# Kernel tuning notes

Measured on AMD Instinct MI355X. Metric: run time of the kernel, lower is better.

## Reference

```python
import jax, jax.numpy as jnp
import numpy as np

NUM_NODES = 10000
NUM_EDGES = 640000
INPUT_DIM = 128
HIDDEN_DIM = 128


def setup_inputs() -> dict:
    key = jax.random.key(0)
    k_x, k_e, k_w1, k_b1, k_w2, k_b2 = jax.random.split(key, 6)
    x = jax.random.normal(k_x, (NUM_NODES, INPUT_DIM), dtype=jnp.float32)
    edge_index = jax.random.randint(k_e, (NUM_EDGES, 2), 0, NUM_NODES, dtype=jnp.int64)
    # MLP params (torch Linear: y = x @ W.T + b; store W already transposed as [in, out])
    s1 = 1.0 / np.sqrt(INPUT_DIM)
    s2 = 1.0 / np.sqrt(HIDDEN_DIM)
    W1 = jax.random.uniform(k_w1, (INPUT_DIM, HIDDEN_DIM), jnp.float32, -s1, s1)
    b1 = jax.random.uniform(k_b1, (HIDDEN_DIM,), jnp.float32, -s1, s1)
    W2 = jax.random.uniform(k_w2, (HIDDEN_DIM, HIDDEN_DIM), jnp.float32, -s2, s2)
    b2 = jax.random.uniform(k_b2, (HIDDEN_DIM,), jnp.float32, -s2, s2)
    return {"x": x, "edge_index": edge_index, "W1": W1, "b1": b1, "W2": W2, "b2": b2}


def reference(x, edge_index, W1, b1, W2, b2):
    # GIN aggregation: sum of neighbor features along edges (row <- col) + self loop.
    row = edge_index[:, 0]
    col = edge_index[:, 1]
    # scatter-add gathered neighbor features into destination nodes
    agg = jax.ops.segment_sum(x[col], row, num_segments=NUM_NODES)
    agg = agg + x  # self-loop contribution (identity edges appended in torch code)
    # 2-layer MLP: Linear -> ReLU -> Linear
    h = jnp.maximum(agg @ W1 + b1, 0.0)
    return h @ W2 + b2
```

## Files before the change

kernel.cpp:

```cpp
#include <hip/hip_runtime.h>

#define NN   10000
#define NE   640000
#define DIM  128
#define NTILES (NN / 16)
#define NBIN  320
#define CAPB  4096
#define EPB   2048
#define FILL_BLOCKS ((NE + EPB - 1) / EPB)
#define CLCAP 512
#define PREP_ITEMS 193088

typedef __attribute__((ext_vector_type(8))) short bf16x8;
typedef __attribute__((ext_vector_type(8))) unsigned short u16x8;
typedef __attribute__((ext_vector_type(4))) float f32x4;

__device__ inline unsigned short f2bf(float f) {
    unsigned u = __builtin_bit_cast(unsigned, f);
    unsigned r = (u + 0x7fffu + ((u >> 16) & 1u)) >> 16;
    return (unsigned short)r;
}
__device__ inline float bf2f(unsigned short u) {
    return __builtin_bit_cast(float, (unsigned)u << 16);
}

#define OFF_BINMEM 1280
#define OFF_XB     5244160
#define OFF_W1P    7804160
#define OFF_W2P    7836928
#define WS_NEED    7869696

__global__ __launch_bounds__(256) void prep_kernel(
        const float* __restrict__ W1, const float* __restrict__ W2,
        const float* __restrict__ x,
        unsigned short* __restrict__ W1p, unsigned short* __restrict__ W2p,
        unsigned short* __restrict__ xb, int* __restrict__ bincnt) {
    int id = blockIdx.x * 256 + threadIdx.x;
    if (id < 32768) {
        const float* W = (id < 16384) ? W1 : W2;
        unsigned short* Wp = (id < 16384) ? W1p : W2p;
        int f = id & 16383;
        int e = f & 7, lane = (f >> 3) & 63, kt = (f >> 9) & 3, nt = f >> 11;
        int kglob = kt * 32 + (lane >> 4) * 8 + e;
        int jglob = nt * 16 + (lane & 15);
        Wp[f] = f2bf(W[kglob * DIM + jglob]);
    } else if (id < 33088) {
        bincnt[id - 32768] = 0;
    } else if (id < PREP_ITEMS) {
        int i = (id - 33088) * 8;
        float4 a = *reinterpret_cast<const float4*>(x + i);
        float4 b = *reinterpret_cast<const float4*>(x + i + 4);
        u16x8 pk;
        pk[0] = f2bf(a.x); pk[1] = f2bf(a.y); pk[2] = f2bf(a.z); pk[3] = f2bf(a.w);
        pk[4] = f2bf(b.x); pk[5] = f2bf(b.y); pk[6] = f2bf(b.z); pk[7] = f2bf(b.w);
        *reinterpret_cast<u16x8*>(xb + i) = pk;
    }
}

__global__ __launch_bounds__(256) void binfill_kernel(
        const int* __restrict__ ei, int* __restrict__ bincnt,
        unsigned* __restrict__ binmem) {
    __shared__ int hist[NBIN];
    __shared__ int base_s[NBIN];
    const int t = threadIdx.x;
    for (int b = t; b < NBIN; b += 256) hist[b] = 0;
    __syncthreads();

    unsigned pk[8];
    int bn[8], rk[8];
    const int e0 = blockIdx.x * EPB;
    #pragma unroll
    for (int i = 0; i < 8; ++i) {
        int idx = e0 + i * 256 + t;
        bn[i] = -1;
        if (idx < NE) {
            int2 rc = *reinterpret_cast<const int2*>(ei + 2 * idx);
            bn[i] = rc.x >> 5;
            pk[i] = ((unsigned)(rc.x & 31) << 14) | (unsigned)rc.y;
            rk[i] = atomicAdd(&hist[bn[i]], 1);
        }
    }
    __syncthreads();
    for (int b = t; b < NBIN; b += 256) {
        int h = hist[b];
        base_s[b] = (h > 0) ? atomicAdd(&bincnt[b], h) : 0;
    }
    __syncthreads();
    #pragma unroll
    for (int i = 0; i < 8; ++i) {
        if (bn[i] >= 0) {
            int pos = base_s[bn[i]] + rk[i];
            if (pos < CAPB)
                binmem[(size_t)bn[i] * CAPB + pos] = pk[i];
        }
    }
}

__global__ __launch_bounds__(256) void gather_mlp_kernel(
        const unsigned short* __restrict__ xb,
        const int* __restrict__ bincnt,
        const unsigned* __restrict__ binmem,
        const unsigned short* __restrict__ W1p,
        const unsigned short* __restrict__ W2p,
        const float* __restrict__ b1,
        const float* __restrict__ b2,
        float* __restrict__ out) {
    __shared__ __align__(16) unsigned short aggs[16][136];
    __shared__ __align__(16) unsigned short hbuf[16][136];
    __shared__ __align__(16) unsigned short clist[16][CLCAP];
    __shared__ int lcnt[16];

    const int row0 = blockIdx.x * 16;
    const int t = threadIdx.x;

    if (t < 16) lcnt[t] = 0;
    __syncthreads();
    {
        const int bin  = blockIdx.x >> 1;
        const int half = blockIdx.x & 1;
        int bc = bincnt[bin];
        bc = (bc > CAPB) ? CAPB : bc;
        const unsigned* bm = binmem + (size_t)bin * CAPB;
        for (int k = t; k < bc; k += 256) {
            unsigned p = bm[k];
            int rl = p >> 14;
            if ((rl >> 4) == half) {
                int n = rl & 15;
                int slot = atomicAdd(&lcnt[n], 1);
                if (slot < CLCAP)
                    clist[n][slot] = (unsigned short)(p & 0x3FFFu);
            }
        }
    }
    __syncthreads();

    {
        const int n = t >> 4, l = t & 15;
        int deg = lcnt[n];
        deg = (deg > CLCAP) ? CLCAP : deg;
        const size_t lo = l * 8;

        float a0[8], a1[8], a2[8], a3[8];
        {
            u16x8 v = *reinterpret_cast<const u16x8*>(xb + (size_t)(row0 + n) * DIM + lo);
            #pragma unroll
            for (int j = 0; j < 8; ++j) { a0[j] = bf2f(v[j]); a1[j] = 0.f; a2[j] = 0.f; a3[j] = 0.f; }
        }
        int k = 0;
        for (; k + 4 <= deg; k += 4) {
            int c0 = clist[n][k + 0];
            int c1 = clist[n][k + 1];
            int c2 = clist[n][k + 2];
            int c3 = clist[n][k + 3];
            u16x8 v0 = *reinterpret_cast<const u16x8*>(xb + (size_t)c0 * DIM + lo);
            u16x8 v1 = *reinterpret_cast<const u16x8*>(xb + (size_t)c1 * DIM + lo);
            u16x8 v2 = *reinterpret_cast<const u16x8*>(xb + (size_t)c2 * DIM + lo);
            u16x8 v3 = *reinterpret_cast<const u16x8*>(xb + (size_t)c3 * DIM + lo);
            #pragma unroll
            for (int j = 0; j < 8; ++j) {
                a0[j] += bf2f(v0[j]);
                a1[j] += bf2f(v1[j]);
                a2[j] += bf2f(v2[j]);
                a3[j] += bf2f(v3[j]);
            }
        }
        for (; k < deg; ++k) {
            int c = clist[n][k];
            u16x8 v = *reinterpret_cast<const u16x8*>(xb + (size_t)c * DIM + lo);
            #pragma unroll
            for (int j = 0; j < 8; ++j) a0[j] += bf2f(v[j]);
        }
        u16x8 pk;
        #pragma unroll
        for (int j = 0; j < 8; ++j) pk[j] = f2bf((a0[j] + a1[j]) + (a2[j] + a3[j]));
        *reinterpret_cast<u16x8*>(&aggs[n][l * 8]) = pk;
    }
    __syncthreads();

    const int wid  = t >> 6;
    const int lane = t & 63;
    const int r16  = lane & 15;
    const int kg   = lane >> 4;
    const int drow = kg * 4;

    bf16x8 af[4];
    #pragma unroll
    for (int kt = 0; kt < 4; ++kt)
        af[kt] = *reinterpret_cast<const bf16x8*>(&aggs[r16][kt * 32 + kg * 8]);

    const f32x4 zero = {0.f, 0.f, 0.f, 0.f};
    f32x4 acc1[2] = {zero, zero};
    #pragma unroll
    for (int kt = 0; kt < 4; ++kt) {
        #pragma unroll
        for (int q = 0; q < 2; ++q) {
            int nt = wid * 2 + q;
            bf16x8 w = *reinterpret_cast<const bf16x8*>(
                W1p + ((nt * 4 + kt) * 64 + lane) * 8);
            acc1[q] = __builtin_amdgcn_mfma_f32_16x16x32_bf16(af[kt], w, acc1[q], 0, 0, 0);
        }
    }
    #pragma unroll
    for (int q = 0; q < 2; ++q) {
        int nt = wid * 2 + q;
        float bv = b1[nt * 16 + r16];
        #pragma unroll
        for (int r = 0; r < 4; ++r) {
            float h = fmaxf(acc1[q][r] + bv, 0.0f);
            hbuf[drow + r][nt * 16 + r16] = f2bf(h);
        }
    }
    __syncthreads();

    bf16x8 hf[4];
    #pragma unroll
    for (int kt = 0; kt < 4; ++kt)
        hf[kt] = *reinterpret_cast<const bf16x8*>(&hbuf[r16][kt * 32 + kg * 8]);

    f32x4 acc2[2] = {zero, zero};
    #pragma unroll
    for (int kt = 0; kt < 4; ++kt) {
        #pragma unroll
        for (int q = 0; q < 2; ++q) {
            int nt = wid * 2 + q;
            bf16x8 w = *reinterpret_cast<const bf16x8*>(
                W2p + ((nt * 4 + kt) * 64 + lane) * 8);
            acc2[q] = __builtin_amdgcn_mfma_f32_16x16x32_bf16(hf[kt], w, acc2[q], 0, 0, 0);
        }
    }
    #pragma unroll
    for (int q = 0; q < 2; ++q) {
        int nt = wid * 2 + q;
        float bv = b2[nt * 16 + r16];
        #pragma unroll
        for (int r = 0; r < 4; ++r)
            out[(size_t)(row0 + drow + r) * DIM + nt * 16 + r16] = acc2[q][r] + bv;
    }
}

__global__ void fb_zero_kernel(int* __restrict__ p, int n) {
    int i = blockIdx.x * blockDim.x + threadIdx.x;
    if (i < n) p[i] = 0;
}
__global__ void fb_count_kernel(const int* __restrict__ ei, int* __restrict__ deg) {
    int e = blockIdx.x * blockDim.x + threadIdx.x;
    if (e < NE) atomicAdd(&deg[ei[2 * e]], 1);
}
__global__ __launch_bounds__(1024) void fb_scan_kernel(const int* __restrict__ deg,
                                                       int* __restrict__ rowptr) {
    __shared__ int wtot[16];
    const int t = threadIdx.x;
    const int base = t * 10;
    int local[10];
    int s = 0;
    #pragma unroll
    for (int i = 0; i < 10; ++i) {
        int v = (base + i < NN) ? deg[base + i] : 0;
        local[i] = s;
        s += v;
    }
    const int mySum = s;
    #pragma unroll
    for (int off = 1; off < 64; off <<= 1) {
        int v = __shfl_up(s, (unsigned)off, 64);
        if ((t & 63) >= off) s += v;
    }
    if ((t & 63) == 63) wtot[t >> 6] = s;
    __syncthreads();
    if (t == 0) {
        int run = 0;
        #pragma unroll
        for (int i = 0; i < 16; ++i) { int v = wtot[i]; wtot[i] = run; run += v; }
    }
    __syncthreads();
    const int ex = wtot[t >> 6] + (s - mySum);
    #pragma unroll
    for (int i = 0; i < 10; ++i)
        if (base + i < NN) rowptr[base + i] = ex + local[i];
    if (t == 1023) rowptr[NN] = ex + mySum;
}
__global__ void fb_fill_kernel(const int* __restrict__ ei, const int* __restrict__ rowptr,
                               int* __restrict__ fill, int* __restrict__ colidx) {
    int e = blockIdx.x * blockDim.x + threadIdx.x;
    if (e < NE) {
        int r = ei[2 * e], c = ei[2 * e + 1];
        colidx[rowptr[r] + atomicAdd(&fill[r], 1)] = c;
    }
}
__global__ __launch_bounds__(128) void fb_gather_kernel(const float* __restrict__ x,
                                                        const int* __restrict__ rowptr,
                                                        const int* __restrict__ colidx,
                                                        float* __restrict__ agg) {
    const int n = blockIdx.x, j = threadIdx.x;
    const int s = rowptr[n], e = rowptr[n + 1];
    float acc = x[(size_t)n * DIM + j];
    float a0 = 0.f, a1 = 0.f, a2 = 0.f, a3 = 0.f;
    int k = s;
    for (; k + 4 <= e; k += 4) {
        a0 += x[(size_t)colidx[k + 0] * DIM + j];
        a1 += x[(size_t)colidx[k + 1] * DIM + j];
        a2 += x[(size_t)colidx[k + 2] * DIM + j];
        a3 += x[(size_t)colidx[k + 3] * DIM + j];
    }
    for (; k < e; ++k) acc += x[(size_t)colidx[k] * DIM + j];
    agg[(size_t)n * DIM + j] = acc + (a0 + a1) + (a2 + a3);
}
__global__ __launch_bounds__(512) void fb_mlp_kernel(
        const float* __restrict__ agg,
        const float* __restrict__ W1, const float* __restrict__ b1,
        const float* __restrict__ W2, const float* __restrict__ b2,
        float* __restrict__ out) {
    __shared__ float w1s[DIM * DIM];
    __shared__ float w2s[DIM * DIM];
    __shared__ float b1s[DIM], b2s[DIM];
    __shared__ float as[4][DIM], hs[4][DIM];
    for (int i = threadIdx.x; i < DIM * DIM; i += blockDim.x) { w1s[i] = W1[i]; w2s[i] = W2[i]; }
    if (threadIdx.x < DIM) { b1s[threadIdx.x] = b1[threadIdx.x]; b2s[threadIdx.x] = b2[threadIdx.x]; }
    __syncthreads();
    const int r = threadIdx.x >> 7, j = threadIdx.x & 127;
    for (int base = blockIdx.x * 4; base < NN; base += gridDim.x * 4) {
        int rowid = base + r;
        as[r][j] = (rowid < NN) ? agg[(size_t)rowid * DIM + j] : 0.0f;
        __syncthreads();
        float acc = b1s[j];
        #pragma unroll 8
        for (int k = 0; k < DIM; ++k) acc = fmaf(as[r][k], w1s[k * DIM + j], acc);
        hs[r][j] = fmaxf(acc, 0.0f);
        __syncthreads();
        float acc2 = b2s[j];
        #pragma unroll 8
        for (int k = 0; k < DIM; ++k) acc2 = fmaf(hs[r][k], w2s[k * DIM + j], acc2);
        if (rowid < NN) out[(size_t)rowid * DIM + j] = acc2;
        __syncthreads();
    }
}

extern "C" void kernel_launch(void* const* d_in, const int* in_sizes, int n_in,
                              void* d_out, int out_size, void* d_ws, size_t ws_size,
                              hipStream_t stream) {
    const float* x  = (const float*)d_in[0];
    const int*   ei = (const int*)d_in[1];
    const float* W1 = (const float*)d_in[2];
    const float* b1 = (const float*)d_in[3];
    const float* W2 = (const float*)d_in[4];
    const float* b2 = (const float*)d_in[5];
    float* out = (float*)d_out;

    if (ws_size >= WS_NEED) {
        char* ws = (char*)d_ws;
        int* bincnt = (int*)ws;
        unsigned* binmem = (unsigned*)(ws + OFF_BINMEM);
        unsigned short* xb  = (unsigned short*)(ws + OFF_XB);
        unsigned short* W1p = (unsigned short*)(ws + OFF_W1P);
        unsigned short* W2p = (unsigned short*)(ws + OFF_W2P);

        prep_kernel<<<(PREP_ITEMS + 255) / 256, 256, 0, stream>>>(
            W1, W2, x, W1p, W2p, xb, bincnt);
        binfill_kernel<<<FILL_BLOCKS, 256, 0, stream>>>(ei, bincnt, binmem);
        gather_mlp_kernel<<<NTILES, 256, 0, stream>>>(
            xb, bincnt, binmem, W1p, W2p, b1, b2, out);
    } else {
        int* wsI    = (int*)d_ws;
        int* deg    = wsI;
        int* fillc  = wsI + 10240;
        int* rowptr = wsI + 20480;
        int* colidx = wsI + 30720;
        const size_t csr_bytes = (size_t)(30720 + NE) * sizeof(int);
        const size_t agg_bytes = (size_t)NN * DIM * sizeof(float);
        float* agg = (ws_size >= csr_bytes + agg_bytes)
                         ? (float*)((char*)d_ws + csr_bytes) : out;

        fb_zero_kernel<<<(20480 + 255) / 256, 256, 0, stream>>>(deg, 20480);
        fb_count_kernel<<<(NE + 255) / 256, 256, 0, stream>>>(ei, deg);
        fb_scan_kernel<<<1, 1024, 0, stream>>>(deg, rowptr);
        fb_fill_kernel<<<(NE + 255) / 256, 256, 0, stream>>>(ei, rowptr, fillc, colidx);
        fb_gather_kernel<<<NN, 128, 0, stream>>>(x, rowptr, colidx, agg);
        fb_mlp_kernel<<<256, 512, 0, stream>>>(agg, W1, b1, W2, b2, out);
    }
}
```

Before: 41.72 us.

## Merge x-to-bf16 conversion into binning kernel, enlarge edges per bin block

```diff
diff --git a/kernel.cpp b/kernel.cpp
--- a/kernel.cpp
+++ b/kernel.cpp
@@ -6,10 +6,12 @@
 #define NTILES (NN / 16)
 #define NBIN  320
 #define CAPB  4096
-#define EPB   2048
+#define EPB   8192
 #define FILL_BLOCKS ((NE + EPB - 1) / EPB)
+#define CONV_THREADS 160000
+#define CONV_BLOCKS ((CONV_THREADS + 255) / 256)
 #define CLCAP 512
-#define PREP_ITEMS 193088
+#define ZW_ITEMS (32768 + NBIN)
 
 typedef __attribute__((ext_vector_type(8))) short bf16x8;
 typedef __attribute__((ext_vector_type(8))) unsigned short u16x8;
@@ -30,11 +32,10 @@
 #define OFF_W2P    7836928
 #define WS_NEED    7869696
 
-__global__ __launch_bounds__(256) void prep_kernel(
+__global__ __launch_bounds__(256) void zw_kernel(
         const float* __restrict__ W1, const float* __restrict__ W2,
-        const float* __restrict__ x,
         unsigned short* __restrict__ W1p, unsigned short* __restrict__ W2p,
-        unsigned short* __restrict__ xb, int* __restrict__ bincnt) {
+        int* __restrict__ bincnt) {
     int id = blockIdx.x * 256 + threadIdx.x;
     if (id < 32768) {
         const float* W = (id < 16384) ? W1 : W2;
@@ -44,54 +45,53 @@
         int kglob = kt * 32 + (lane >> 4) * 8 + e;
         int jglob = nt * 16 + (lane & 15);
         Wp[f] = f2bf(W[kglob * DIM + jglob]);
-    } else if (id < 33088) {
+    } else if (id < ZW_ITEMS) {
         bincnt[id - 32768] = 0;
-    } else if (id < PREP_ITEMS) {
-        int i = (id - 33088) * 8;
-        float4 a = *reinterpret_cast<const float4*>(x + i);
-        float4 b = *reinterpret_cast<const float4*>(x + i + 4);
-        u16x8 pk;
-        pk[0] = f2bf(a.x); pk[1] = f2bf(a.y); pk[2] = f2bf(a.z); pk[3] = f2bf(a.w);
-        pk[4] = f2bf(b.x); pk[5] = f2bf(b.y); pk[6] = f2bf(b.z); pk[7] = f2bf(b.w);
-        *reinterpret_cast<u16x8*>(xb + i) = pk;
-    }
-}
-
-__global__ __launch_bounds__(256) void binfill_kernel(
-        const int* __restrict__ ei, int* __restrict__ bincnt,
-        unsigned* __restrict__ binmem) {
-    __shared__ int hist[NBIN];
-    __shared__ int base_s[NBIN];
+    }
+}
+
+__global__ __launch_bounds__(256) void build_kernel(
+        const int* __restrict__ ei, const float* __restrict__ x,
+        int* __restrict__ bincnt, unsigned* __restrict__ binmem,
+        unsigned short* __restrict__ xb) {
     const int t = threadIdx.x;
-    for (int b = t; b < NBIN; b += 256) hist[b] = 0;
-    __syncthreads();
-
-    unsigned pk[8];
-    int bn[8], rk[8];
-    const int e0 = blockIdx.x * EPB;
-    #pragma unroll
-    for (int i = 0; i < 8; ++i) {
-        int idx = e0 + i * 256 + t;
-        bn[i] = -1;
-        if (idx < NE) {
-            int2 rc = *reinterpret_cast<const int2*>(ei + 2 * idx);
-            bn[i] = rc.x >> 5;
-            pk[i] = ((unsigned)(rc.x & 31) << 14) | (unsigned)rc.y;
-            rk[i] = atomicAdd(&hist[bn[i]], 1);
-        }
-    }
-    __syncthreads();
-    for (int b = t; b < NBIN; b += 256) {
-        int h = hist[b];
-        base_s[b] = (h > 0) ? atomicAdd(&bincnt[b], h) : 0;
-    }
-    __syncthreads();
-    #pragma unroll
-    for (int i = 0; i < 8; ++i) {
-        if (bn[i] >= 0) {
-            int pos = base_s[bn[i]] + rk[i];
-            if (pos < CAPB)
-                binmem[(size_t)bn[i] * CAPB + pos] = pk[i];
+    if (blockIdx.x < FILL_BLOCKS) {
+        __shared__ int hist[NBIN];
+        for (int b = t; b < NBIN; b += 256) hist[b] = 0;
+        __syncthreads();
+        const int e0 = blockIdx.x * EPB;
+        for (int i = 0; i < EPB / 256; ++i) {
+            int idx = e0 + i * 256 + t;
+            if (idx < NE)
+                atomicAdd(&hist[ei[2 * idx] >> 5], 1);
+        }
+        __syncthreads();
+        for (int b = t; b < NBIN; b += 256) {
+            int h = hist[b];
+            hist[b] = (h > 0) ? atomicAdd(&bincnt[b], h) : 0;
+        }
+        __syncthreads();
+        for (int i = 0; i < EPB / 256; ++i) {
+            int idx = e0 + i * 256 + t;
+            if (idx < NE) {
+                int2 rc = *reinterpret_cast<const int2*>(ei + 2 * idx);
+                int bn = rc.x >> 5;
+                int pos = atomicAdd(&hist[bn], 1);
+                if (pos < CAPB)
+                    binmem[(size_t)bn * CAPB + pos] =
+                        ((unsigned)(rc.x & 31) << 14) | (unsigned)rc.y;
+            }
+        }
+    } else {
+        int pid = (blockIdx.x - FILL_BLOCKS) * 256 + t;
+        if (pid < CONV_THREADS) {
+            int i = pid * 8;
+            float4 a = *reinterpret_cast<const float4*>(x + i);
+            float4 b = *reinterpret_cast<const float4*>(x + i + 4);
+            u16x8 pk;
+            pk[0] = f2bf(a.x); pk[1] = f2bf(a.y); pk[2] = f2bf(a.z); pk[3] = f2bf(a.w);
+            pk[4] = f2bf(b.x); pk[5] = f2bf(b.y); pk[6] = f2bf(b.z); pk[7] = f2bf(b.w);
+            *reinterpret_cast<u16x8*>(xb + i) = pk;
         }
     }
 }
@@ -354,9 +354,10 @@
         unsigned short* W1p = (unsigned short*)(ws + OFF_W1P);
         unsigned short* W2p = (unsigned short*)(ws + OFF_W2P);
 
-        prep_kernel<<<(PREP_ITEMS + 255) / 256, 256, 0, stream>>>(
-            W1, W2, x, W1p, W2p, xb, bincnt);
-        binfill_kernel<<<FILL_BLOCKS, 256, 0, stream>>>(ei, bincnt, binmem);
+        zw_kernel<<<(ZW_ITEMS + 255) / 256, 256, 0, stream>>>(
+            W1, W2, W1p, W2p, bincnt);
+        build_kernel<<<FILL_BLOCKS + CONV_BLOCKS, 256, 0, stream>>>(
+            ei, x, bincnt, binmem, xb);
         gather_mlp_kernel<<<NTILES, 256, 0, stream>>>(
             xb, bincnt, binmem, W1p, W2p, b1, b2, out);
     } else {
```

Measured after the change: 50.24 us. 1.2x slower.
